# Kernel optimization log

Hardware: AMD Instinct MI355X
Metric: run time of the kernel (lower is better)

Reference implementation:

```python
import jax, jax.numpy as jnp
import numpy as np

N_TOK, D_MODEL, N_EXPERTS, TOP_K = 8192, 512, 8, 2


def setup_inputs() -> dict:
    key = jax.random.key(0)
    k1, k2, k3 = jax.random.split(key, 3)
    x = jax.random.normal(k1, (N_TOK, D_MODEL), jnp.float32)
    w_gate = jax.random.normal(k2, (D_MODEL, N_EXPERTS), jnp.float32) * 0.02
    expert_w = jax.random.normal(k3, (N_EXPERTS, D_MODEL, D_MODEL), jnp.float32) * (D_MODEL ** -0.5)
    return {"x": x, "w_gate": w_gate, "expert_w": expert_w, "top_k": TOP_K}


def _cv_sq(v):
    m = jnp.mean(v)
    return jnp.var(v) / (m * m + 1e-10)


def reference(x, w_gate, expert_w, top_k):
    # ---- Gate (clean top-k gating, eval mode of noisy-top-k) ----
    logits = x @ w_gate                              # [N, E]
    top_vals, top_idx = jax.lax.top_k(logits, top_k)  # [N, k]
    top_gates = jax.nn.softmax(top_vals, axis=-1)
    n, e = logits.shape
    gates = jnp.zeros((n, e), x.dtype).at[jnp.arange(n)[:, None], top_idx].set(top_gates)

    # ---- dispatch -> per-expert GEMM -> log-domain combine ----
    # combine(): stitched = cat(expert_out).exp() * nonzero_gates; index_add over
    # batch index; zeros -> eps; log. Dense-equivalent (tokens with gate 0
    # contribute exactly nothing):
    expert_out = jnp.einsum('nd,edf->nef', x, expert_w)   # per-expert outputs [N, E, D]
    combined = jnp.einsum('ne,nef->nf', gates, jnp.exp(expert_out))  # [N, D]
    eps = np.float32(np.finfo(np.float64).eps)
    combined = jnp.where(combined == 0, eps, combined)
    out = jnp.log(combined)

    # ---- load-balance aux loss: cv^2(importance) + cv^2(load) ----
    importance = gates.sum(0)
    load = (gates > 0).sum(0).astype(x.dtype)
    balance_loss = _cv_sq(importance) + _cv_sq(load)
    return out, balance_loss
```

## Files before the change

kernel.cpp:

```cpp
#include <hip/hip_runtime.h>
#include <hip/hip_bf16.h>
#include <math.h>

#define N_TOK 8192
#define D 512
#define NE 8

typedef float f32x4 __attribute__((ext_vector_type(4)));
typedef __bf16 bf16x8 __attribute__((ext_vector_type(8)));
typedef unsigned short u16;
typedef u16 u16x8 __attribute__((ext_vector_type(8)));

#define OFF_TOKE  256
#define OFF_TOKG  65792
#define OFF_BUCK  131328
#define OFF_XB    (1u << 20)
#define OFF_EWT   (OFF_XB + 8u * 1024 * 1024)
#define OFF_Y     (OFF_EWT + 4u * 1024 * 1024)

__device__ __forceinline__ u16 f2b(float v) {
    __hip_bfloat16 h = __float2bfloat16(v);
    return *reinterpret_cast<u16*>(&h);
}
__device__ __forceinline__ float b2f(u16 u) {
    __hip_bfloat16 h;
    *reinterpret_cast<u16*>(&h) = u;
    return __bfloat162float(h);
}

typedef __attribute__((address_space(1))) const void* gp1_t;
typedef __attribute__((address_space(3))) void* lp3_t;
__device__ __forceinline__ void gload16(const void* g, void* l) {
    __builtin_amdgcn_global_load_lds((gp1_t)g, (lp3_t)l, 16, 0, 0);
}

__global__ __launch_bounds__(256) void gate_prep_kernel(
    const float* __restrict__ x, const float* __restrict__ wg,
    const float* __restrict__ ew,
    int* __restrict__ tok_e, float* __restrict__ tok_g, u16* __restrict__ xb,
    u16* __restrict__ ewt)
{
    __shared__ __align__(16) float sbuf[64 * 65];
    int b = blockIdx.x;
    int tid = threadIdx.x;

    if (b >= 2048) {
        int pb = b - 2048;
        float (*tile)[65] = (float(*)[65])sbuf;
        int e = pb >> 6, dt = (pb >> 3) & 7, ftl = pb & 7;
        int c = tid & 63, rq = tid >> 6;
        const float* src = ew + (size_t)e * D * D + (size_t)(dt * 64) * D + ftl * 64;
#pragma unroll
        for (int i = 0; i < 16; ++i) {
            int r = i * 4 + rq;
            tile[r][c] = src[(size_t)r * D + c];
        }
        __syncthreads();
        u16* dst = ewt + (size_t)e * D * D + (size_t)(ftl * 64) * D + dt * 64;
#pragma unroll
        for (int i = 0; i < 16; ++i) {
            int f = i * 4 + rq;
            dst[(size_t)f * D + c] = f2b(tile[c][f]);
        }
        return;
    }

    float* wgs = sbuf;
    for (int i = tid; i < NE * D; i += 256) {
        int d = i >> 3, e = i & 7;
        wgs[e * D + d] = wg[i];
    }
    __syncthreads();

    int wave = tid >> 6, lane = tid & 63;
    int n = b * 4 + wave;
    const float* xr = x + (size_t)n * D;
    u16* xbr = xb + (size_t)n * D;

    float p[NE];
#pragma unroll
    for (int e = 0; e < NE; ++e) p[e] = 0.f;
#pragma unroll
    for (int it = 0; it < 8; ++it) {
        float xv = xr[it * 64 + lane];
        xbr[it * 64 + lane] = f2b(xv);
#pragma unroll
        for (int e = 0; e < NE; ++e)
            p[e] += xv * wgs[e * D + it * 64 + lane];
    }
#pragma unroll
    for (int off = 32; off > 0; off >>= 1) {
#pragma unroll
        for (int e = 0; e < NE; ++e)
            p[e] += __shfl_xor(p[e], off);
    }

    if (lane == 0) {
        int e1 = 0; float v1 = p[0];
#pragma unroll
        for (int e = 1; e < NE; ++e) if (p[e] > v1) { v1 = p[e]; e1 = e; }
        int e2 = -1; float v2 = -INFINITY;
#pragma unroll
        for (int e = 0; e < NE; ++e) if (e != e1 && p[e] > v2) { v2 = p[e]; e2 = e; }
        float t = __expf(v2 - v1);
        float inv = 1.f / (1.f + t);
        tok_e[2 * n] = e1;     tok_e[2 * n + 1] = e2;
        tok_g[2 * n] = inv;    tok_g[2 * n + 1] = t * inv;
    }
}

__global__ __launch_bounds__(256) void bucketize_kernel(
    const int* __restrict__ tok_e, const float* __restrict__ tok_g,
    int* __restrict__ count, float* __restrict__ imp, int* __restrict__ bucket)
{
    __shared__ int lcnt[NE], lbase[NE];
    __shared__ float limp[NE];
    int tid = threadIdx.x;
    if (tid < NE) { lcnt[tid] = 0; limp[tid] = 0.f; }
    __syncthreads();

    int n = blockIdx.x * 256 + tid;
    int e1 = tok_e[2 * n], e2 = tok_e[2 * n + 1];
    float g1 = tok_g[2 * n], g2 = tok_g[2 * n + 1];
    int o1 = atomicAdd(&lcnt[e1], 1);
    int o2 = atomicAdd(&lcnt[e2], 1);
    atomicAdd(&limp[e1], g1);
    atomicAdd(&limp[e2], g2);
    __syncthreads();
    if (tid < NE) {
        lbase[tid] = atomicAdd(&count[tid], lcnt[tid]);
        atomicAdd(&imp[tid], limp[tid]);
    }
    __syncthreads();
    bucket[e1 * N_TOK + lbase[e1] + o1] = 2 * n;
    bucket[e2 * N_TOK + lbase[e2] + o2] = 2 * n + 1;
}

__global__ __launch_bounds__(256) void moe_gemm(
    const u16* __restrict__ xb, const u16* __restrict__ ewt,
    const int* __restrict__ count, const int* __restrict__ bucket,
    u16* __restrict__ y)
{
    int b = blockIdx.x;
    int ft = b & 3;
    int tt = (b >> 2) & 63;
    int e  = b >> 8;
    int cnt = count[e];
    if (tt * 128 >= cnt) return;

    __shared__ int sl[128];
    __shared__ __align__(16) u16 smem[16384];

    int tid = threadIdx.x;
    if (tid < 128) {
        int idx = tt * 128 + tid;
        sl[tid] = (idx < cnt) ? bucket[e * N_TOK + idx] : -1;
    }
    __syncthreads();

    int w = tid >> 6, l = tid & 63;
    int c8 = (l & 3) * 8;
    int r0 = w * 32 + (l >> 2);
    int r1 = r0 + 16;
    int s0 = sl[r0], s1 = sl[r1];
    int ta0 = (s0 < 0) ? 0 : (s0 >> 1);
    int ta1 = (s1 < 0) ? 0 : (s1 >> 1);
    const u16* gA0 = xb + (size_t)ta0 * D + c8;
    const u16* gA1 = xb + (size_t)ta1 * D + c8;
    const u16* gB0 = ewt + ((size_t)e * D + ft * 128 + r0) * D + c8;
    const u16* gB1 = ewt + ((size_t)e * D + ft * 128 + r1) * D + c8;

    int wm = w & 1, wn = w >> 1;
    int lm = l & 15, quad = l >> 4, kq = quad * 8;

    f32x4 acc[4][4] = {};

    auto stage = [&](int p, int kc) {
        u16* As = smem + p * 8192;
        u16* Bs = As + 4096;
        gload16(gA0 + kc * 32, &As[(w * 32) * 32]);
        gload16(gA1 + kc * 32, &As[(w * 32 + 16) * 32]);
        gload16(gB0 + kc * 32, &Bs[(w * 32) * 32]);
        gload16(gB1 + kc * 32, &Bs[(w * 32 + 16) * 32]);
    };

    stage(0, 0);
    int cur = 0;
    for (int kc = 0; kc < 16; ++kc) {
        if (kc < 15) {
            stage(cur ^ 1, kc + 1);
            asm volatile("s_waitcnt vmcnt(4)" ::: "memory");
        } else {
            asm volatile("s_waitcnt vmcnt(0)" ::: "memory");
        }
        __builtin_amdgcn_s_barrier();
        asm volatile("" ::: "memory");

        const u16* As = smem + cur * 8192;
        const u16* Bs = As + 4096;
        bf16x8 af[4], bfv[4];
#pragma unroll
        for (int i = 0; i < 4; ++i)
            af[i] = *(const bf16x8*)&As[(wm * 64 + i * 16 + lm) * 32 + kq];
#pragma unroll
        for (int j = 0; j < 4; ++j)
            bfv[j] = *(const bf16x8*)&Bs[(wn * 64 + j * 16 + lm) * 32 + kq];
#pragma unroll
        for (int i = 0; i < 4; ++i)
#pragma unroll
            for (int j = 0; j < 4; ++j)
                acc[i][j] = __builtin_amdgcn_mfma_f32_16x16x32_bf16(
                    af[i], bfv[j], acc[i][j], 0, 0, 0);

        asm volatile("s_waitcnt lgkmcnt(0)" ::: "memory");
        __builtin_amdgcn_s_barrier();
        cur ^= 1;
    }

    __syncthreads();
    u16* Es = smem + w * 2304;
#pragma unroll
    for (int h = 0; h < 2; ++h) {
#pragma unroll
        for (int i2 = 0; i2 < 2; ++i2) {
            int i = h * 2 + i2;
#pragma unroll
            for (int j = 0; j < 4; ++j)
#pragma unroll
                for (int r = 0; r < 4; ++r)
                    Es[(i2 * 16 + quad * 4 + r) * 72 + j * 16 + lm] =
                        f2b(acc[i][j][r]);
        }
        int row = l >> 1, hc = l & 1;
        int s = sl[wm * 64 + h * 32 + row];
        const u16* src = Es + row * 72 + hc * 32;
        u16* dst = y + (size_t)((s < 0) ? 0 : s) * D + ft * 128 + wn * 64 + hc * 32;
        if (s >= 0) {
#pragma unroll
            for (int c = 0; c < 4; ++c)
                *(u16x8*)(dst + c * 8) = *(const u16x8*)(src + c * 8);
        }
        __syncthreads();
    }
}

__global__ __launch_bounds__(256) void combine_kernel(
    const u16* __restrict__ y, const float* __restrict__ tok_g,
    const int* __restrict__ count, const float* __restrict__ imp,
    float* __restrict__ out)
{
    if (blockIdx.x == 4096) {
        if (threadIdx.x == 0) {
            float mi = 0.f, ml = 0.f;
            for (int e = 0; e < NE; ++e) { mi += imp[e]; ml += (float)count[e]; }
            mi *= 0.125f; ml *= 0.125f;
            float vi = 0.f, vl = 0.f;
            for (int e = 0; e < NE; ++e) {
                float di = imp[e] - mi;          vi += di * di;
                float dl = (float)count[e] - ml; vl += dl * dl;
            }
            vi *= 0.125f; vl *= 0.125f;
            out[N_TOK * D] = vi / (mi * mi + 1e-10f) + vl / (ml * ml + 1e-10f);
        }
        return;
    }
    int idx = blockIdx.x * 256 + threadIdx.x;
    int n = idx >> 7;
    int c = (idx & 127) * 4;
    const ushort4 ua = *(const ushort4*)(y + (size_t)(2 * n) * D + c);
    const ushort4 ub = *(const ushort4*)(y + (size_t)(2 * n + 1) * D + c);
    float g1 = tok_g[2 * n], g2 = tok_g[2 * n + 1];
    const float eps = 2.2204460492503131e-16f;
    float4 r;
    float v;
    v = g1 * __expf(b2f(ua.x)) + g2 * __expf(b2f(ub.x)); r.x = __logf(v == 0.f ? eps : v);
    v = g1 * __expf(b2f(ua.y)) + g2 * __expf(b2f(ub.y)); r.y = __logf(v == 0.f ? eps : v);
    v = g1 * __expf(b2f(ua.z)) + g2 * __expf(b2f(ub.z)); r.z = __logf(v == 0.f ? eps : v);
    v = g1 * __expf(b2f(ua.w)) + g2 * __expf(b2f(ub.w)); r.w = __logf(v == 0.f ? eps : v);
    *(float4*)(out + (size_t)n * D + c) = r;
}

extern "C" void kernel_launch(void* const* d_in, const int* in_sizes, int n_in,
                              void* d_out, int out_size, void* d_ws, size_t ws_size,
                              hipStream_t stream)
{
    const float* x  = (const float*)d_in[0];
    const float* wg = (const float*)d_in[1];
    const float* ew = (const float*)d_in[2];
    char* ws = (char*)d_ws;
    int*   count  = (int*)(ws + 0);
    float* imp    = (float*)(ws + 64);
    int*   tok_e  = (int*)(ws + OFF_TOKE);
    float* tok_g  = (float*)(ws + OFF_TOKG);
    int*   bucket = (int*)(ws + OFF_BUCK);
    u16*   xb     = (u16*)(ws + OFF_XB);
    u16*   ewt    = (u16*)(ws + OFF_EWT);
    u16*   y      = (u16*)(ws + OFF_Y);
    float* out    = (float*)d_out;

    hipMemsetAsync(ws, 0, 128, stream);
    gate_prep_kernel<<<2048 + 512, 256, 0, stream>>>(x, wg, ew, tok_e, tok_g, xb, ewt);
    bucketize_kernel<<<N_TOK / 256, 256, 0, stream>>>(tok_e, tok_g, count, imp, bucket);
    moe_gemm<<<NE * 64 * 4, 256, 0, stream>>>(xb, ewt, count, bucket, y);
    combine_kernel<<<4097, 256, 0, stream>>>(y, tok_g, count, imp, out);
}
```

Before: 123.7 us.

## Triple-buffer MoE GEMM with single barrier; widen gate and combine per-thread work

The expert GEMM moves from double to triple LDS buffering, prefetching two K-chunks ahead. It needs only one barrier per iteration and raises wave priority around the MFMA block. The gate kernel now processes four tokens per wave with float4 loads, which amortises the per-block gate-weight staging. The combine kernel handles eight elements per thread with 16-byte loads. The trade-off is more LDS per GEMM block, which may lower occupancy.

Result: faster. 119.5 us, median of 2 (-3.4%).

```diff
diff --git a/kernel.cpp b/kernel.cpp
--- a/kernel.cpp
+++ b/kernel.cpp
@@ -44,8 +44,8 @@
     int b = blockIdx.x;
     int tid = threadIdx.x;
 
-    if (b >= 2048) {
-        int pb = b - 2048;
+    if (b >= 512) {
+        int pb = b - 512;
         float (*tile)[65] = (float(*)[65])sbuf;
         int e = pb >> 6, dt = (pb >> 3) & 7, ftl = pb & 7;
         int c = tid & 63, rq = tid >> 6;
@@ -73,39 +73,46 @@
     __syncthreads();
 
     int wave = tid >> 6, lane = tid & 63;
-    int n = b * 4 + wave;
-    const float* xr = x + (size_t)n * D;
-    u16* xbr = xb + (size_t)n * D;
-
-    float p[NE];
-#pragma unroll
-    for (int e = 0; e < NE; ++e) p[e] = 0.f;
-#pragma unroll
-    for (int it = 0; it < 8; ++it) {
-        float xv = xr[it * 64 + lane];
-        xbr[it * 64 + lane] = f2b(xv);
-#pragma unroll
-        for (int e = 0; e < NE; ++e)
-            p[e] += xv * wgs[e * D + it * 64 + lane];
-    }
-#pragma unroll
-    for (int off = 32; off > 0; off >>= 1) {
-#pragma unroll
-        for (int e = 0; e < NE; ++e)
-            p[e] += __shfl_xor(p[e], off);
-    }
-
-    if (lane == 0) {
-        int e1 = 0; float v1 = p[0];
-#pragma unroll
-        for (int e = 1; e < NE; ++e) if (p[e] > v1) { v1 = p[e]; e1 = e; }
-        int e2 = -1; float v2 = -INFINITY;
-#pragma unroll
-        for (int e = 0; e < NE; ++e) if (e != e1 && p[e] > v2) { v2 = p[e]; e2 = e; }
-        float t = __expf(v2 - v1);
-        float inv = 1.f / (1.f + t);
-        tok_e[2 * n] = e1;     tok_e[2 * n + 1] = e2;
-        tok_g[2 * n] = inv;    tok_g[2 * n + 1] = t * inv;
+#pragma unroll
+    for (int t = 0; t < 4; ++t) {
+        int n = b * 16 + wave * 4 + t;
+        const float4* xr4 = (const float4*)(x + (size_t)n * D);
+        ushort4* xb4 = (ushort4*)(xb + (size_t)n * D);
+
+        float p[NE];
+#pragma unroll
+        for (int e = 0; e < NE; ++e) p[e] = 0.f;
+#pragma unroll
+        for (int it = 0; it < 2; ++it) {
+            float4 v = xr4[it * 64 + lane];
+            ushort4 s;
+            s.x = f2b(v.x); s.y = f2b(v.y); s.z = f2b(v.z); s.w = f2b(v.w);
+            xb4[it * 64 + lane] = s;
+#pragma unroll
+            for (int e = 0; e < NE; ++e) {
+                float4 wv = *(const float4*)&wgs[e * D + (it * 64 + lane) * 4];
+                p[e] += v.x * wv.x + v.y * wv.y + v.z * wv.z + v.w * wv.w;
+            }
+        }
+#pragma unroll
+        for (int off = 32; off > 0; off >>= 1) {
+#pragma unroll
+            for (int e = 0; e < NE; ++e)
+                p[e] += __shfl_xor(p[e], off);
+        }
+
+        if (lane == 0) {
+            int e1 = 0; float v1 = p[0];
+#pragma unroll
+            for (int e = 1; e < NE; ++e) if (p[e] > v1) { v1 = p[e]; e1 = e; }
+            int e2 = -1; float v2 = -INFINITY;
+#pragma unroll
+            for (int e = 0; e < NE; ++e) if (e != e1 && p[e] > v2) { v2 = p[e]; e2 = e; }
+            float tv = __expf(v2 - v1);
+            float inv = 1.f / (1.f + tv);
+            tok_e[2 * n] = e1;     tok_e[2 * n + 1] = e2;
+            tok_g[2 * n] = inv;    tok_g[2 * n + 1] = tv * inv;
+        }
     }
 }
 
@@ -149,7 +156,7 @@
     if (tt * 128 >= cnt) return;
 
     __shared__ int sl[128];
-    __shared__ __align__(16) u16 smem[16384];
+    __shared__ __align__(16) u16 smem[24576];
 
     int tid = threadIdx.x;
     if (tid < 128) {
@@ -185,19 +192,25 @@
     };
 
     stage(0, 0);
-    int cur = 0;
+    stage(1, 1);
+    int bi = 0, bj = 2;
     for (int kc = 0; kc < 16; ++kc) {
-        if (kc < 15) {
-            stage(cur ^ 1, kc + 1);
-            asm volatile("s_waitcnt vmcnt(4)" ::: "memory");
-        } else {
-            asm volatile("s_waitcnt vmcnt(0)" ::: "memory");
-        }
+        if (kc < 15)
+            asm volatile("s_waitcnt vmcnt(4) lgkmcnt(0)" ::: "memory");
+        else
+            asm volatile("s_waitcnt vmcnt(0) lgkmcnt(0)" ::: "memory");
         __builtin_amdgcn_s_barrier();
         asm volatile("" ::: "memory");
 
-        const u16* As = smem + cur * 8192;
+        if (kc < 14) {
+            stage(bj, kc + 2);
+            bj = (bj == 2) ? 0 : bj + 1;
+        }
+
+        const u16* As = smem + bi * 8192;
         const u16* Bs = As + 4096;
+        bi = (bi == 2) ? 0 : bi + 1;
+
         bf16x8 af[4], bfv[4];
 #pragma unroll
         for (int i = 0; i < 4; ++i)
@@ -205,16 +218,15 @@
 #pragma unroll
         for (int j = 0; j < 4; ++j)
             bfv[j] = *(const bf16x8*)&Bs[(wn * 64 + j * 16 + lm) * 32 + kq];
+
+        __builtin_amdgcn_s_setprio(1);
 #pragma unroll
         for (int i = 0; i < 4; ++i)
 #pragma unroll
             for (int j = 0; j < 4; ++j)
                 acc[i][j] = __builtin_amdgcn_mfma_f32_16x16x32_bf16(
                     af[i], bfv[j], acc[i][j], 0, 0, 0);
-
-        asm volatile("s_waitcnt lgkmcnt(0)" ::: "memory");
-        __builtin_amdgcn_s_barrier();
-        cur ^= 1;
+        __builtin_amdgcn_s_setprio(0);
     }
 
     __syncthreads();
@@ -249,7 +261,7 @@
     const int* __restrict__ count, const float* __restrict__ imp,
     float* __restrict__ out)
 {
-    if (blockIdx.x == 4096) {
+    if (blockIdx.x == 2048) {
         if (threadIdx.x == 0) {
             float mi = 0.f, ml = 0.f;
             for (int e = 0; e < NE; ++e) { mi += imp[e]; ml += (float)count[e]; }
@@ -265,19 +277,21 @@
         return;
     }
     int idx = blockIdx.x * 256 + threadIdx.x;
-    int n = idx >> 7;
-    int c = (idx & 127) * 4;
-    const ushort4 ua = *(const ushort4*)(y + (size_t)(2 * n) * D + c);
-    const ushort4 ub = *(const ushort4*)(y + (size_t)(2 * n + 1) * D + c);
+    int n = idx >> 6;
+    int c = (idx & 63) * 8;
+    const u16x8 ua = *(const u16x8*)(y + (size_t)(2 * n) * D + c);
+    const u16x8 ub = *(const u16x8*)(y + (size_t)(2 * n + 1) * D + c);
     float g1 = tok_g[2 * n], g2 = tok_g[2 * n + 1];
     const float eps = 2.2204460492503131e-16f;
-    float4 r;
-    float v;
-    v = g1 * __expf(b2f(ua.x)) + g2 * __expf(b2f(ub.x)); r.x = __logf(v == 0.f ? eps : v);
-    v = g1 * __expf(b2f(ua.y)) + g2 * __expf(b2f(ub.y)); r.y = __logf(v == 0.f ? eps : v);
-    v = g1 * __expf(b2f(ua.z)) + g2 * __expf(b2f(ub.z)); r.z = __logf(v == 0.f ? eps : v);
-    v = g1 * __expf(b2f(ua.w)) + g2 * __expf(b2f(ub.w)); r.w = __logf(v == 0.f ? eps : v);
-    *(float4*)(out + (size_t)n * D + c) = r;
+    float r[8];
+#pragma unroll
+    for (int k = 0; k < 8; ++k) {
+        float v = g1 * __expf(b2f(ua[k])) + g2 * __expf(b2f(ub[k]));
+        r[k] = __logf(v == 0.f ? eps : v);
+    }
+    float* o = out + (size_t)n * D + c;
+    *(float4*)o       = make_float4(r[0], r[1], r[2], r[3]);
+    *(float4*)(o + 4) = make_float4(r[4], r[5], r[6], r[7]);
 }
 
 extern "C" void kernel_launch(void* const* d_in, const int* in_sizes, int n_in,
@@ -299,8 +313,8 @@
     float* out    = (float*)d_out;
 
     hipMemsetAsync(ws, 0, 128, stream);
-    gate_prep_kernel<<<2048 + 512, 256, 0, stream>>>(x, wg, ew, tok_e, tok_g, xb, ewt);
+    gate_prep_kernel<<<512 + 512, 256, 0, stream>>>(x, wg, ew, tok_e, tok_g, xb, ewt);
     bucketize_kernel<<<N_TOK / 256, 256, 0, stream>>>(tok_e, tok_g, count, imp, bucket);
     moe_gemm<<<NE * 64 * 4, 256, 0, stream>>>(xb, ewt, count, bucket, y);
-    combine_kernel<<<4097, 256, 0, stream>>>(y, tok_g, count, imp, out);
-}
+    combine_kernel<<<2049, 256, 0, stream>>>(y, tok_g, count, imp, out);
+}
```
